# Optimization experiments

Hardware: AMD Instinct MI355X
Metric: run time of the kernel (lower is better)

## Reference

```python
import jax, jax.numpy as jnp
import numpy as np

KNN = 5
SEARCH = 3
CUTOFF = 1.0
NCLASSES = 21
D, H, W = 32, 128, 2048
P = 1048576


def setup_inputs() -> dict:
    key = jax.random.key(0)
    k1, k2, k3, k4, k5, k6 = jax.random.split(key, 6)
    proj_range = jax.random.uniform(k1, (D, H, W), dtype=jnp.float32)
    unproj_range = jax.random.uniform(k2, (P,), dtype=jnp.float32)
    proj_argmax = jax.random.randint(k3, (D, H, W), 0, NCLASSES).astype(jnp.int32)
    px = jax.random.randint(k4, (P,), 0, W).astype(jnp.int32)
    py = jax.random.randint(k5, (P,), 0, H).astype(jnp.int32)
    pz = jax.random.randint(k6, (P,), 0, D).astype(jnp.int32)
    return {"proj_range": proj_range, "unproj_range": unproj_range,
            "proj_argmax": proj_argmax, "px": px, "py": py, "pz": pz}


def reference(proj_range, unproj_range, proj_argmax, px, py, pz):
    pad = (SEARCH - 1) // 2
    k3 = SEARCH ** 3
    center = (k3 - 1) // 2  # = 13 for search=3
    n_pts = unproj_range.shape[0]

    # zero padding replicates F.unfold's implicit zero pad (padded entries stay 0,
    # which is NOT mapped to inf by the `< 0` mask, matching the torch code)
    pr_pad = jnp.pad(proj_range, pad)
    pa_pad = jnp.pad(proj_argmax, pad)

    # kernel offsets, flattened in (dz, dy, dx) order like unfoldNd
    offs = jnp.arange(SEARCH, dtype=jnp.int32)
    oz, oy, ox = jnp.meshgrid(offs, offs, offs, indexing="ij")
    oz, oy, ox = oz.reshape(-1), oy.reshape(-1), ox.reshape(-1)  # [k3]

    # per-point neighborhood indices into the padded volume: [P, k3]
    zi = pz[:, None] + oz[None, :]
    yi = py[:, None] + oy[None, :]
    xi = px[:, None] + ox[None, :]

    nb_rang = pr_pad[zi, yi, xi]                       # [P, k3]
    nb_rang = jnp.where(nb_rang < 0, jnp.inf, nb_rang)
    nb_rang = nb_rang.at[:, center].set(unproj_range)  # center = query range

    k2_dist = jnp.abs(nb_rang - unproj_range[:, None])  # [P, k3]

    neg_top, knn_idx = jax.lax.top_k(-k2_dist, KNN)     # smallest-k distances
    knn_dist = -neg_top                                  # [P, KNN]

    nb_arg = pa_pad[zi, yi, xi]                          # [P, k3] int
    knn_arg = jnp.take_along_axis(nb_arg, knn_idx, axis=1)
    knn_arg = jnp.where(knn_dist > CUTOFF, NCLASSES, knn_arg)  # cutoff -> invalid class

    # scatter-add voting over classes 0..NCLASSES
    counts = jnp.zeros((n_pts, NCLASSES + 1), dtype=proj_range.dtype)
    counts = counts.at[jnp.arange(n_pts, dtype=jnp.int32)[:, None], knn_arg].add(1.0)

    # argmax over classes 1..NCLASSES-1 (drop class 0 and invalid bucket), then +1
    out = jnp.argmax(counts[:, 1:-1], axis=1).astype(jnp.int32) + 1
    return out
```

## Files before the change

kernel.cpp:

```cpp
#include <hip/hip_runtime.h>
#include <math.h>

#define KNN 5
#define K3 27
#define CENTER 13
#define NCLASSES 21
#define DIM_D 32
#define DIM_H 128
#define DIM_W 2048

#define RADIX 256
#define BIN_PTS 2048
#define SEG_TILE 2048


typedef float    float4u __attribute__((ext_vector_type(4), aligned(4)));
typedef int      int4u   __attribute__((ext_vector_type(4), aligned(4)));
typedef unsigned uint2u  __attribute__((ext_vector_type(2), aligned(4)));
typedef unsigned uint4e  __attribute__((ext_vector_type(4), aligned(16)));

#define SENTINEL 3.0e38f
#define BITS_TWO 0x4000000000000000ULL

__device__ __forceinline__ unsigned seg_of_xy(int x, int y) {
    return ((unsigned)y << 1) | ((unsigned)x >> 10);
}
__device__ __forceinline__ unsigned seg_of_wy(unsigned wy) {
    return (((wy >> 11) & 0x7Fu) << 1) | ((wy >> 10) & 1u);
}
__device__ __forceinline__ unsigned b8_of_wy(unsigned wy) {
    return (((wy >> 18) & 31u) << 3) | ((wy >> 7) & 7u);
}

__global__ __launch_bounds__(256) void pack_pa_kernel(
    const int4* __restrict__ pa, uchar4* __restrict__ out, int n4)
{
    int i = blockIdx.x * 256 + threadIdx.x;
    if (i < n4) {
        int4 v = pa[i];
        out[i] = make_uchar4((unsigned char)v.x, (unsigned char)v.y,
                             (unsigned char)v.z, (unsigned char)v.w);
    }
}

__global__ __launch_bounds__(256) void hist0_kernel(
    const int* __restrict__ px, const int* __restrict__ py,
    unsigned* __restrict__ h0, int P)
{
    __shared__ unsigned lh0[RADIX];
    int t = threadIdx.x;
    lh0[t] = 0;
    __syncthreads();
    int base4 = blockIdx.x * 1024 + t;
#pragma unroll
    for (int g = 0; g < 4; ++g) {
        int i4 = base4 + g * 256;
        int i0 = i4 * 4;
        if (i0 + 3 < P) {
            int4 X = ((const int4*)px)[i4];
            int4 Y = ((const int4*)py)[i4];
            atomicAdd(&lh0[seg_of_xy(X.x, Y.x)], 1u);
            atomicAdd(&lh0[seg_of_xy(X.y, Y.y)], 1u);
            atomicAdd(&lh0[seg_of_xy(X.z, Y.z)], 1u);
            atomicAdd(&lh0[seg_of_xy(X.w, Y.w)], 1u);
        } else {
            for (int i = i0; i < P; ++i)
                atomicAdd(&lh0[seg_of_xy(px[i], py[i])], 1u);
        }
    }
    __syncthreads();
    if (lh0[t]) atomicAdd(&h0[t], lh0[t]);
}

__global__ __launch_bounds__(256) void scan256_dup_kernel(
    unsigned* __restrict__ h, unsigned* __restrict__ hbase)
{
    __shared__ unsigned ws[4];
    int t = threadIdx.x, lane = t & 63, wid = t >> 6;
    unsigned a = h[t], ia = a;
#pragma unroll
    for (int off = 1; off < 64; off <<= 1) {
        unsigned v = __shfl_up(ia, off);
        if (lane >= off) ia += v;
    }
    if (lane == 63) ws[wid] = ia;
    __syncthreads();
    unsigned b = 0;
#pragma unroll
    for (int w = 0; w < 4; ++w) b += (w < wid) ? ws[w] : 0u;
    unsigned excl = b + ia - a;
    h[t] = excl;
    hbase[t] = excl;
}

struct BinShared {
    unsigned lh[RADIX];
    unsigned lscan[RADIX];
    unsigned gbase[RADIX];
    unsigned wsum[4];
    uint4 stage[BIN_PTS];
};

__global__ __launch_bounds__(512) void bin_pass1_kernel(
    const float* __restrict__ ur, const int* __restrict__ px,
    const int* __restrict__ py, const int* __restrict__ pz,
    unsigned* __restrict__ g0, uint4* __restrict__ outp, int P)
{
    __shared__ BinShared S;
    int t = threadIdx.x, lane = t & 63, wid = t >> 6;
    int bstart = blockIdx.x * BIN_PTS;
    int n = min(BIN_PTS, P - bstart);
    if (t < RADIX) S.lh[t] = 0;
    __syncthreads();

    uint4 pay[4];
    unsigned rk[4], dg[4];
    {
        int i4 = (bstart >> 2) + t;
        int i0 = i4 * 4;
        if (i0 + 3 < P) {
            int4 X = ((const int4*)px)[i4];
            int4 Y = ((const int4*)py)[i4];
            int4 Z = ((const int4*)pz)[i4];
            float4 U = ((const float4*)ur)[i4];
            int xs[4] = {X.x, X.y, X.z, X.w};
            int ys[4] = {Y.x, Y.y, Y.z, Y.w};
            int zs[4] = {Z.x, Z.y, Z.z, Z.w};
            float us[4] = {U.x, U.y, U.z, U.w};
#pragma unroll
            for (int c = 0; c < 4; ++c) {
                dg[c] = seg_of_xy(xs[c], ys[c]);
                rk[c] = atomicAdd(&S.lh[dg[c]], 1u);
                pay[c] = make_uint4(__float_as_uint(us[c]),
                    (unsigned)xs[c] | ((unsigned)ys[c] << 11) | ((unsigned)zs[c] << 18),
                    (unsigned)(i0 + c), 0u);
            }
        } else {
#pragma unroll
            for (int c = 0; c < 4; ++c) {
                int gi = i0 + c;
                if (gi < P) {
                    int x = px[gi], y = py[gi], z = pz[gi];
                    dg[c] = seg_of_xy(x, y);
                    rk[c] = atomicAdd(&S.lh[dg[c]], 1u);
                    pay[c] = make_uint4(__float_as_uint(ur[gi]),
                        (unsigned)x | ((unsigned)y << 11) | ((unsigned)z << 18),
                        (unsigned)gi, 0u);
                } else {
                    dg[c] = 0xFFFFFFFFu;
                }
            }
        }
    }
    __syncthreads();

    {
        unsigned c0 = (t < RADIX) ? S.lh[t] : 0u;
        unsigned inc = c0;
#pragma unroll
        for (int off = 1; off < 64; off <<= 1) {
            unsigned v = __shfl_up(inc, off);
            if (lane >= off) inc += v;
        }
        if (t < RADIX && lane == 63) S.wsum[wid] = inc;
        __syncthreads();
        if (t < RADIX) {
            unsigned wb = 0;
#pragma unroll
            for (int w = 0; w < 4; ++w) wb += (w < wid) ? S.wsum[w] : 0u;
            S.lscan[t] = wb + inc - c0;
            S.gbase[t] = c0 ? atomicAdd(&g0[t], c0) : 0u;
        }
    }
    __syncthreads();
#pragma unroll
    for (int c = 0; c < 4; ++c)
        if (dg[c] != 0xFFFFFFFFu)
            S.stage[S.lscan[dg[c]] + rk[c]] = pay[c];
    __syncthreads();
#pragma unroll
    for (int j = 0; j < 4; ++j) {
        int s = j * 512 + t;
        if (s < n) {
            uint4 v = S.stage[s];
            unsigned d = seg_of_wy(v.y);
            unsigned pos = S.gbase[d] + ((unsigned)s - S.lscan[d]);
            outp[pos] = v;
        }
    }
}

__global__ __launch_bounds__(1024) void pass2b_kernel(
    const uint4* __restrict__ inp, const unsigned* __restrict__ segBase,
    uint4* __restrict__ outp, int P)
{
    __shared__ unsigned bh[RADIX];
    __shared__ unsigned cur[RADIX];
    __shared__ unsigned lz[RADIX];
    __shared__ unsigned lsc[RADIX];
    __shared__ unsigned wsum[4];
    __shared__ uint4 stage[SEG_TILE];

    int b = blockIdx.x;
    unsigned s0 = segBase[b];
    unsigned s1 = (b == RADIX - 1) ? (unsigned)P : segBase[b + 1];
    int t = threadIdx.x, lane = t & 63, wid = t >> 6;

    if (t < RADIX) bh[t] = 0;
    __syncthreads();

    for (unsigned i = s0 + t; i < s1; i += 1024)
        atomicAdd(&bh[b8_of_wy(inp[i].y)], 1u);
    __syncthreads();

    {
        unsigned c0 = (t < RADIX) ? bh[t] : 0u;
        unsigned inc = c0;
#pragma unroll
        for (int off = 1; off < 64; off <<= 1) {
            unsigned v = __shfl_up(inc, off);
            if (lane >= off) inc += v;
        }
        if (t < RADIX && lane == 63) wsum[wid] = inc;
        __syncthreads();
        if (t < RADIX) {
            unsigned wb = 0;
#pragma unroll
            for (int w = 0; w < 4; ++w) wb += (w < wid) ? wsum[w] : 0u;
            cur[t] = s0 + wb + inc - c0;
        }
    }
    __syncthreads();

    for (unsigned tb = s0; tb < s1; tb += SEG_TILE) {
        unsigned m = min((unsigned)SEG_TILE, s1 - tb);
        if (t < RADIX) lz[t] = 0;
        __syncthreads();
        uint4 pay[2];
        unsigned rk[2], zz[2];
#pragma unroll
        for (int j = 0; j < 2; ++j) {
            int s = j * 1024 + t;
            if (s < (int)m) {
                uint4 v = inp[tb + (unsigned)s];
                pay[j] = v;
                zz[j] = b8_of_wy(v.y);
                rk[j] = atomicAdd(&lz[zz[j]], 1u);
            } else {
                zz[j] = 0xFFFFFFFFu;
            }
        }
        __syncthreads();
        {
            unsigned c0 = (t < RADIX) ? lz[t] : 0u;
            unsigned inc = c0;
#pragma unroll
            for (int off = 1; off < 64; off <<= 1) {
                unsigned v = __shfl_up(inc, off);
                if (lane >= off) inc += v;
            }
            if (t < RADIX && lane == 63) wsum[wid] = inc;
            __syncthreads();
            if (t < RADIX) {
                unsigned wb = 0;
#pragma unroll
                for (int w = 0; w < 4; ++w) wb += (w < wid) ? wsum[w] : 0u;
                lsc[t] = wb + inc - c0;
            }
        }
        __syncthreads();
#pragma unroll
        for (int j = 0; j < 2; ++j)
            if (zz[j] != 0xFFFFFFFFu)
                stage[lsc[zz[j]] + rk[j]] = pay[j];
        __syncthreads();
#pragma unroll
        for (int j = 0; j < 2; ++j) {
            int s = j * 1024 + t;
            if (s < (int)m) {
                uint4 v = stage[s];
                unsigned d = b8_of_wy(v.y);
                outp[cur[d] + ((unsigned)s - lsc[d])] = v;
            }
        }
        __syncthreads();
        if (t < RADIX) cur[t] += lz[t];
        __syncthreads();
    }
}

template <bool U8>
__device__ __forceinline__ void bev_knn_body(
    const float* __restrict__ pr, const int* __restrict__ pa,
    const unsigned char* __restrict__ pa8,
    float u, int x, int y, int z, int oidx, int* __restrict__ out)
{
    int xo = min(max(x - 1, 0), DIM_W - 4);
    int s = x - 1 - xo;
    int xo8 = (max(x - 1, 0)) & ~3;
    int sb = (x - 1) - xo8;

    float4u L[9];
    int4u   A[9];
    uint2u  B[9];
    bool okr[9];
#pragma unroll
    for (int r = 0; r < 9; ++r) {
        const int dz = r / 3 - 1;
        const int dy = r % 3 - 1;
        int zz = z + dz, yy = y + dy;
        bool ok = ((unsigned)zz < (unsigned)DIM_D) &
                  ((unsigned)yy < (unsigned)DIM_H);
        okr[r] = ok;
        int row = ok ? (zz * DIM_H + yy) : 0;
        size_t rb = ((size_t)row) << 11;
        L[r] = *(const float4u*)(pr + rb + xo);
        if (U8) B[r] = *(const uint2u*)(pa8 + rb + xo8);
        else    A[r] = *(const int4u*)(pa + rb + xo);
    }

    double bd[KNN];
#pragma unroll
    for (int j = 0; j < KNN; ++j) bd[j] = 1.0e308;

    auto push = [&](int k, float v, unsigned cls) {
        float d = fabsf(v - u);
        d = (v < 0.f) ? SENTINEL : d;
        if (k == CENTER) d = 0.0f;
        double key = (double)d + 1.0;
        unsigned long long kb =
            (unsigned long long)__double_as_longlong(key)
            | (unsigned long long)(((unsigned)k << 5) | (cls & 31u));
        double kd = __longlong_as_double((long long)kb);
#pragma unroll
        for (int j = 0; j < KNN; ++j) {
            double lo = fmin(bd[j], kd);
            kd = fmax(bd[j], kd);
            bd[j] = lo;
        }
    };

    bool fast = __all(s == 0);
    if (fast) {
#pragma unroll
        for (int r = 0; r < 9; ++r) {
            bool ok = okr[r];
            float v0, v1, v2;
            unsigned cc0, cc1, cc2;
            v0 = ok ? L[r].x : 0.f;
            v1 = ok ? L[r].y : 0.f;
            v2 = ok ? L[r].z : 0.f;
            if (U8) {
                unsigned long long v64 =
                    ((unsigned long long)B[r].y << 32) | B[r].x;
                unsigned c3 = ok ? (unsigned)(v64 >> (8 * sb)) : 0u;
                cc0 = c3 & 0xFFu;
                cc1 = (c3 >> 8) & 0xFFu;
                cc2 = (c3 >> 16) & 0xFFu;
            } else {
                cc0 = ok ? (unsigned)A[r].x : 0u;
                cc1 = ok ? (unsigned)A[r].y : 0u;
                cc2 = ok ? (unsigned)A[r].z : 0u;
            }
            push(r * 3 + 0, v0, cc0);
            push(r * 3 + 1, v1, cc1);
            push(r * 3 + 2, v2, cc2);
        }
    } else {
#pragma unroll
        for (int r = 0; r < 9; ++r) {
            bool ok = okr[r];
            float a0 = ok ? L[r].x : 0.f;
            float a1 = ok ? L[r].y : 0.f;
            float a2 = ok ? L[r].z : 0.f;
            float a3 = ok ? L[r].w : 0.f;
            float v0 = (s == 0) ? a0 : ((s == -1) ? 0.f : ((s == 1) ? a1 : a2));
            float v1 = (s == 0) ? a1 : ((s == -1) ? a0 : ((s == 1) ? a2 : a3));
            float v2 = (s == 0) ? a2 : ((s == -1) ? a1 : ((s == 1) ? a3 : 0.f));
            unsigned cv[3];
            if (U8) {
                unsigned long long v64 = ok ?
                    (((unsigned long long)B[r].y << 32) | B[r].x) : 0ULL;
#pragma unroll
                for (int j = 0; j < 3; ++j) {
                    int xm = x - 1 + j;
                    bool xv = (unsigned)xm < (unsigned)DIM_W;
                    int idx = sb + j;
                    idx = idx < 0 ? 0 : idx;
                    unsigned byte = (unsigned)((v64 >> (8 * idx)) & 0xFFu);
                    cv[j] = xv ? byte : 0u;
                }
            } else {
                unsigned c0 = ok ? (unsigned)A[r].x : 0u;
                unsigned c1 = ok ? (unsigned)A[r].y : 0u;
                unsigned c2 = ok ? (unsigned)A[r].z : 0u;
                unsigned c3 = ok ? (unsigned)A[r].w : 0u;
                cv[0] = (s == 0) ? c0 : ((s == -1) ? 0u : ((s == 1) ? c1 : c2));
                cv[1] = (s == 0) ? c1 : ((s == -1) ? c0 : ((s == 1) ? c2 : c3));
                cv[2] = (s == 0) ? c2 : ((s == -1) ? c1 : ((s == 1) ? c3 : 0u));
            }
            push(r * 3 + 0, v0, cv[0]);
            push(r * 3 + 1, v1, cv[1]);
            push(r * 3 + 2, v2, cv[2]);
        }
    }

    int votes[KNN];
#pragma unroll
    for (int j = 0; j < KNN; ++j) {
        unsigned long long kb =
            (unsigned long long)__double_as_longlong(bd[j]);
        int cls = (int)(kb & 31u);
        bool cut = (kb & ~1023ULL) > BITS_TWO;
        votes[j] = cut ? NCLASSES : cls;
    }

    int best_cnt = 0, best_cls = 1;
#pragma unroll
    for (int j = 0; j < KNN; ++j) {
        int v = votes[j];
        if (v >= 1 && v <= NCLASSES - 1) {
            int cnt = 0;
#pragma unroll
            for (int i = 0; i < KNN; ++i) cnt += (votes[i] == v) ? 1 : 0;
            if (cnt > best_cnt || (cnt == best_cnt && v < best_cls)) {
                best_cnt = cnt;
                best_cls = v;
            }
        }
    }
    __builtin_nontemporal_store(best_cls, &out[oidx]);
}

__device__ __forceinline__ int swizzle_block(int b, int nb) {
    if ((nb & 7) == 0) {
        int per = nb >> 3;
        return (b & 7) * per + (b >> 3);
    }
    return b;
}

template <bool U8>
__global__ __launch_bounds__(256) void bev_knn_aos_kernel(
    const float* __restrict__ pr, const int* __restrict__ pa,
    const unsigned char* __restrict__ pa8,
    const uint4* __restrict__ payload, int* __restrict__ out, int P)
{
    int lb = swizzle_block(blockIdx.x, gridDim.x);
    int p = lb * blockDim.x + threadIdx.x;
    if (p >= P) return;
    uint4e w = __builtin_nontemporal_load((const uint4e*)(payload + p));
    float u = __uint_as_float(w.x);
    int x = (int)(w.y & 0x7FFu);
    int y = (int)((w.y >> 11) & 0x7Fu);
    int z = (int)((w.y >> 18) & 0x1Fu);
    bev_knn_body<U8>(pr, pa, pa8, u, x, y, z, (int)w.z, out);
}

__global__ __launch_bounds__(256) void bev_knn_direct_kernel(
    const float* __restrict__ pr, const int* __restrict__ pa,
    const float* __restrict__ ur, const int* __restrict__ px,
    const int* __restrict__ py, const int* __restrict__ pz,
    int* __restrict__ out, int P)
{
    int p = blockIdx.x * blockDim.x + threadIdx.x;
    if (p >= P) return;
    bev_knn_body<false>(pr, pa, (const unsigned char*)nullptr,
                        ur[p], px[p], py[p], pz[p], p, out);
}

extern "C" void kernel_launch(void* const* d_in, const int* in_sizes, int n_in,
                              void* d_out, int out_size, void* d_ws, size_t ws_size,
                              hipStream_t stream) {
    const float* pr = (const float*)d_in[0];
    const float* ur = (const float*)d_in[1];
    const int*   pa = (const int*)d_in[2];
    const int*   px = (const int*)d_in[3];
    const int*   py = (const int*)d_in[4];
    const int*   pz = (const int*)d_in[5];
    int* out = (int*)d_out;
    int P = in_sizes[1];
    int gridH = (P + 4095) / 4096;
    int gridB = (P + BIN_PTS - 1) / BIN_PTS;
    int gridD = (P + 255) / 256;

    const int VOXELS = DIM_D * DIM_H * DIM_W;
    size_t h_b    = (size_t)RADIX * 4;
    size_t hb_b   = (size_t)RADIX * 4;
    size_t p_off  = (h_b + hb_b + 15) & ~(size_t)15;
    size_t pay_b  = (size_t)P * 16;
    size_t need   = p_off + 2 * pay_b;
    size_t pack_b = ((size_t)VOXELS + 31) & ~(size_t)31;
    size_t need8  = need + pack_b;

    if (ws_size >= need) {
        char* ws = (char*)d_ws;
        unsigned* h0cur  = (unsigned*)ws;
        unsigned* h0base = (unsigned*)(ws + h_b);
        uint4*    pay1   = (uint4*)(ws + p_off);
        uint4*    pay2   = (uint4*)(ws + p_off + pay_b);
        unsigned char* pa8 = (unsigned char*)(ws + p_off + 2 * pay_b);
        bool use8 = (ws_size >= need8);

        hipMemsetAsync(h0cur, 0, h_b, stream);
        if (use8) {
            int n4 = VOXELS / 4;
            pack_pa_kernel<<<(n4 + 255) / 256, 256, 0, stream>>>(
                (const int4*)pa, (uchar4*)pa8, n4);
        }
        hist0_kernel<<<gridH, 256, 0, stream>>>(px, py, h0cur, P);
        scan256_dup_kernel<<<1, 256, 0, stream>>>(h0cur, h0base);
        bin_pass1_kernel<<<gridB, 512, 0, stream>>>(ur, px, py, pz,
                                                    h0cur, pay1, P);
        pass2b_kernel<<<RADIX, 1024, 0, stream>>>(pay1, h0base, pay2, P);
        if (use8)
            bev_knn_aos_kernel<true><<<gridD, 256, 0, stream>>>(
                pr, pa, pa8, pay2, out, P);
        else
            bev_knn_aos_kernel<false><<<gridD, 256, 0, stream>>>(
                pr, pa, nullptr, pay2, out, P);
    } else {
        bev_knn_direct_kernel<<<gridD, 256, 0, stream>>>(pr, pa, ur, px, py,
                                                         pz, out, P);
    }
}
```

Measured before the change: 180.5 us.

## Fuse pack, histogram and scan into one kernel; precompute second-level bin counts

Merges the int-to-byte argmax packing, the first-level segment histogram and the 256-entry scan into a single prep kernel. A last-block-done atomic counter runs the scan, which removes two kernel launches. The first binning pass now also builds the second-level 256x256 histogram with global atomics, so pass2b no longer rereads its whole segment just to count sub-bins. The cost is one global atomic per point on a 256 KB count table and a larger workspace memset.

```diff
diff --git a/kernel.cpp b/kernel.cpp
--- a/kernel.cpp
+++ b/kernel.cpp
@@ -32,65 +32,70 @@
     return (((wy >> 18) & 31u) << 3) | ((wy >> 7) & 7u);
 }
 
-__global__ __launch_bounds__(256) void pack_pa_kernel(
-    const int4* __restrict__ pa, uchar4* __restrict__ out, int n4)
+__global__ __launch_bounds__(256) void prep_kernel(
+    const int4* __restrict__ pa, uchar4* __restrict__ pa8,
+    const int* __restrict__ px, const int* __restrict__ py,
+    unsigned* __restrict__ h0, unsigned* __restrict__ hbase,
+    unsigned* __restrict__ done, int n4, int P, int histBlocks)
 {
-    int i = blockIdx.x * 256 + threadIdx.x;
+    __shared__ unsigned lh0[RADIX];
+    __shared__ unsigned sws[4];
+    __shared__ bool isLast;
+    int t = threadIdx.x;
+    int b = blockIdx.x;
+
+    int i = b * 256 + t;
     if (i < n4) {
         int4 v = pa[i];
-        out[i] = make_uchar4((unsigned char)v.x, (unsigned char)v.y,
+        pa8[i] = make_uchar4((unsigned char)v.x, (unsigned char)v.y,
                              (unsigned char)v.z, (unsigned char)v.w);
     }
-}
-
-__global__ __launch_bounds__(256) void hist0_kernel(
-    const int* __restrict__ px, const int* __restrict__ py,
-    unsigned* __restrict__ h0, int P)
-{
-    __shared__ unsigned lh0[RADIX];
-    int t = threadIdx.x;
-    lh0[t] = 0;
-    __syncthreads();
-    int base4 = blockIdx.x * 1024 + t;
-#pragma unroll
-    for (int g = 0; g < 4; ++g) {
-        int i4 = base4 + g * 256;
-        int i0 = i4 * 4;
-        if (i0 + 3 < P) {
-            int4 X = ((const int4*)px)[i4];
-            int4 Y = ((const int4*)py)[i4];
-            atomicAdd(&lh0[seg_of_xy(X.x, Y.x)], 1u);
-            atomicAdd(&lh0[seg_of_xy(X.y, Y.y)], 1u);
-            atomicAdd(&lh0[seg_of_xy(X.z, Y.z)], 1u);
-            atomicAdd(&lh0[seg_of_xy(X.w, Y.w)], 1u);
-        } else {
-            for (int i = i0; i < P; ++i)
-                atomicAdd(&lh0[seg_of_xy(px[i], py[i])], 1u);
-        }
-    }
-    __syncthreads();
-    if (lh0[t]) atomicAdd(&h0[t], lh0[t]);
-}
-
-__global__ __launch_bounds__(256) void scan256_dup_kernel(
-    unsigned* __restrict__ h, unsigned* __restrict__ hbase)
-{
-    __shared__ unsigned ws[4];
-    int t = threadIdx.x, lane = t & 63, wid = t >> 6;
-    unsigned a = h[t], ia = a;
-#pragma unroll
-    for (int off = 1; off < 64; off <<= 1) {
-        unsigned v = __shfl_up(ia, off);
-        if (lane >= off) ia += v;
-    }
-    if (lane == 63) ws[wid] = ia;
-    __syncthreads();
-    unsigned b = 0;
-#pragma unroll
-    for (int w = 0; w < 4; ++w) b += (w < wid) ? ws[w] : 0u;
-    unsigned excl = b + ia - a;
-    h[t] = excl;
-    hbase[t] = excl;
+
+    if (b < histBlocks) {
+        lh0[t] = 0;
+        __syncthreads();
+        int base4 = b * 1024 + t;
+#pragma unroll
+        for (int g = 0; g < 4; ++g) {
+            int i4 = base4 + g * 256;
+            int i0 = i4 * 4;
+            if (i0 + 3 < P) {
+                int4 X = ((const int4*)px)[i4];
+                int4 Y = ((const int4*)py)[i4];
+                atomicAdd(&lh0[seg_of_xy(X.x, Y.x)], 1u);
+                atomicAdd(&lh0[seg_of_xy(X.y, Y.y)], 1u);
+                atomicAdd(&lh0[seg_of_xy(X.z, Y.z)], 1u);
+                atomicAdd(&lh0[seg_of_xy(X.w, Y.w)], 1u);
+            } else {
+                for (int j = i0; j < P; ++j)
+                    atomicAdd(&lh0[seg_of_xy(px[j], py[j])], 1u);
+            }
+        }
+        __syncthreads();
+        if (lh0[t]) atomicAdd(&h0[t], lh0[t]);
+    }
+
+    __syncthreads();
+    if (t == 0)
+        isLast = (atomicAdd(done, 1u) == (unsigned)(gridDim.x - 1));
+    __syncthreads();
+    if (isLast) {
+        int lane = t & 63, wid = t >> 6;
+        unsigned a = atomicAdd(&h0[t], 0u), ia = a;
+#pragma unroll
+        for (int off = 1; off < 64; off <<= 1) {
+            unsigned v = __shfl_up(ia, off);
+            if (lane >= off) ia += v;
+        }
+        if (lane == 63) sws[wid] = ia;
+        __syncthreads();
+        unsigned bb = 0;
+#pragma unroll
+        for (int w = 0; w < 4; ++w) bb += (w < wid) ? sws[w] : 0u;
+        unsigned excl = bb + ia - a;
+        h0[t] = excl;
+        hbase[t] = excl;
+    }
 }
 
 struct BinShared {
@@ -104,7 +109,8 @@
 __global__ __launch_bounds__(512) void bin_pass1_kernel(
     const float* __restrict__ ur, const int* __restrict__ px,
     const int* __restrict__ py, const int* __restrict__ pz,
-    unsigned* __restrict__ g0, uint4* __restrict__ outp, int P)
+    unsigned* __restrict__ g0, unsigned* __restrict__ cnt16,
+    uint4* __restrict__ outp, int P)
 {
     __shared__ BinShared S;
     int t = threadIdx.x, lane = t & 63, wid = t >> 6;
@@ -134,6 +140,7 @@
                 pay[c] = make_uint4(__float_as_uint(us[c]),
                     (unsigned)xs[c] | ((unsigned)ys[c] << 11) | ((unsigned)zs[c] << 18),
                     (unsigned)(i0 + c), 0u);
+                atomicAdd(&cnt16[(dg[c] << 8) | b8_of_wy(pay[c].y)], 1u);
             }
         } else {
 #pragma unroll
@@ -146,6 +153,7 @@
                     pay[c] = make_uint4(__float_as_uint(ur[gi]),
                         (unsigned)x | ((unsigned)y << 11) | ((unsigned)z << 18),
                         (unsigned)gi, 0u);
+                    atomicAdd(&cnt16[(dg[c] << 8) | b8_of_wy(pay[c].y)], 1u);
                 } else {
                     dg[c] = 0xFFFFFFFFu;
                 }
@@ -192,9 +200,8 @@
 
 __global__ __launch_bounds__(1024) void pass2b_kernel(
     const uint4* __restrict__ inp, const unsigned* __restrict__ segBase,
-    uint4* __restrict__ outp, int P)
+    const unsigned* __restrict__ cnt16, uint4* __restrict__ outp, int P)
 {
-    __shared__ unsigned bh[RADIX];
     __shared__ unsigned cur[RADIX];
     __shared__ unsigned lz[RADIX];
     __shared__ unsigned lsc[RADIX];
@@ -206,15 +213,8 @@
     unsigned s1 = (b == RADIX - 1) ? (unsigned)P : segBase[b + 1];
     int t = threadIdx.x, lane = t & 63, wid = t >> 6;
 
-    if (t < RADIX) bh[t] = 0;
-    __syncthreads();
-
-    for (unsigned i = s0 + t; i < s1; i += 1024)
-        atomicAdd(&bh[b8_of_wy(inp[i].y)], 1u);
-    __syncthreads();
-
     {
-        unsigned c0 = (t < RADIX) ? bh[t] : 0u;
+        unsigned c0 = (t < RADIX) ? cnt16[(b << 8) | t] : 0u;
         unsigned inc = c0;
 #pragma unroll
         for (int off = 1; off < 64; off <<= 1) {
@@ -480,16 +480,18 @@
     const int*   pz = (const int*)d_in[5];
     int* out = (int*)d_out;
     int P = in_sizes[1];
-    int gridH = (P + 4095) / 4096;
     int gridB = (P + BIN_PTS - 1) / BIN_PTS;
     int gridD = (P + 255) / 256;
+    int histBlocks = (P + 4095) / 4096;
 
     const int VOXELS = DIM_D * DIM_H * DIM_W;
     size_t h_b    = (size_t)RADIX * 4;
     size_t hb_b   = (size_t)RADIX * 4;
-    size_t p_off  = (h_b + hb_b + 15) & ~(size_t)15;
+    size_t done_b = 16;
+    size_t cnt_b  = (size_t)RADIX * RADIX * 4;
+    size_t pre    = (h_b + hb_b + done_b + cnt_b + 255) & ~(size_t)255;
     size_t pay_b  = (size_t)P * 16;
-    size_t need   = p_off + 2 * pay_b;
+    size_t need   = pre + 2 * pay_b;
     size_t pack_b = ((size_t)VOXELS + 31) & ~(size_t)31;
     size_t need8  = need + pack_b;
 
@@ -497,22 +499,25 @@
         char* ws = (char*)d_ws;
         unsigned* h0cur  = (unsigned*)ws;
         unsigned* h0base = (unsigned*)(ws + h_b);
-        uint4*    pay1   = (uint4*)(ws + p_off);
-        uint4*    pay2   = (uint4*)(ws + p_off + pay_b);
-        unsigned char* pa8 = (unsigned char*)(ws + p_off + 2 * pay_b);
+        unsigned* done   = (unsigned*)(ws + h_b + hb_b);
+        unsigned* cnt16  = (unsigned*)(ws + h_b + hb_b + done_b);
+        uint4*    pay1   = (uint4*)(ws + pre);
+        uint4*    pay2   = (uint4*)(ws + pre + pay_b);
+        unsigned char* pa8 = (unsigned char*)(ws + pre + 2 * pay_b);
         bool use8 = (ws_size >= need8);
 
-        hipMemsetAsync(h0cur, 0, h_b, stream);
-        if (use8) {
-            int n4 = VOXELS / 4;
-            pack_pa_kernel<<<(n4 + 255) / 256, 256, 0, stream>>>(
-                (const int4*)pa, (uchar4*)pa8, n4);
-        }
-        hist0_kernel<<<gridH, 256, 0, stream>>>(px, py, h0cur, P);
-        scan256_dup_kernel<<<1, 256, 0, stream>>>(h0cur, h0base);
+        hipMemsetAsync(ws, 0, pre, stream);
+
+        int n4 = use8 ? (VOXELS / 4) : 0;
+        int packBlocks = use8 ? (n4 + 255) / 256 : 0;
+        int gridP = max(packBlocks, histBlocks);
+        prep_kernel<<<gridP, 256, 0, stream>>>(
+            (const int4*)pa, (uchar4*)pa8, px, py,
+            h0cur, h0base, done, n4, P, histBlocks);
         bin_pass1_kernel<<<gridB, 512, 0, stream>>>(ur, px, py, pz,
-                                                    h0cur, pay1, P);
-        pass2b_kernel<<<RADIX, 1024, 0, stream>>>(pay1, h0base, pay2, P);
+                                                    h0cur, cnt16, pay1, P);
+        pass2b_kernel<<<RADIX, 1024, 0, stream>>>(pay1, h0base, cnt16,
+                                                  pay2, P);
         if (use8)
             bev_knn_aos_kernel<true><<<gridD, 256, 0, stream>>>(
                 pr, pa, pa8, pay2, out, P);
```

Result: slower. 293.8 us (+62.8%).

## Convert sorted point payload from padded AoS uint4 to three SoA arrays

Applied to the files above, without the earlier changes.

The 16-byte per-point payload (range, packed xyz, index, unused pad) is replaced by three separate 4-byte arrays across both binning passes and the KNN kernel. This drops the unused fourth word, cutting intermediate payload traffic by a quarter, and gives coalesced 4-byte accesses. The cost is three separate scattered stores per point instead of one 16-byte store, plus more LDS staging arrays and extra memory instructions. The workspace layout is adjusted to match.

```diff
diff --git a/kernel.cpp b/kernel.cpp
--- a/kernel.cpp
+++ b/kernel.cpp
@@ -17,7 +17,6 @@
 typedef float    float4u __attribute__((ext_vector_type(4), aligned(4)));
 typedef int      int4u   __attribute__((ext_vector_type(4), aligned(4)));
 typedef unsigned uint2u  __attribute__((ext_vector_type(2), aligned(4)));
-typedef unsigned uint4e  __attribute__((ext_vector_type(4), aligned(16)));
 
 #define SENTINEL 3.0e38f
 #define BITS_TWO 0x4000000000000000ULL
@@ -98,13 +97,17 @@
     unsigned lscan[RADIX];
     unsigned gbase[RADIX];
     unsigned wsum[4];
-    uint4 stage[BIN_PTS];
+    unsigned stW[BIN_PTS];
+    unsigned stU[BIN_PTS];
+    unsigned stI[BIN_PTS];
 };
 
 __global__ __launch_bounds__(512) void bin_pass1_kernel(
     const float* __restrict__ ur, const int* __restrict__ px,
     const int* __restrict__ py, const int* __restrict__ pz,
-    unsigned* __restrict__ g0, uint4* __restrict__ outp, int P)
+    unsigned* __restrict__ g0,
+    unsigned* __restrict__ oW, unsigned* __restrict__ oU,
+    unsigned* __restrict__ oI, int P)
 {
     __shared__ BinShared S;
     int t = threadIdx.x, lane = t & 63, wid = t >> 6;
@@ -113,8 +116,7 @@
     if (t < RADIX) S.lh[t] = 0;
     __syncthreads();
 
-    uint4 pay[4];
-    unsigned rk[4], dg[4];
+    unsigned pw[4], pu[4], rk[4], dg[4];
     {
         int i4 = (bstart >> 2) + t;
         int i0 = i4 * 4;
@@ -131,9 +133,9 @@
             for (int c = 0; c < 4; ++c) {
                 dg[c] = seg_of_xy(xs[c], ys[c]);
                 rk[c] = atomicAdd(&S.lh[dg[c]], 1u);
-                pay[c] = make_uint4(__float_as_uint(us[c]),
-                    (unsigned)xs[c] | ((unsigned)ys[c] << 11) | ((unsigned)zs[c] << 18),
-                    (unsigned)(i0 + c), 0u);
+                pw[c] = (unsigned)xs[c] | ((unsigned)ys[c] << 11)
+                        | ((unsigned)zs[c] << 18);
+                pu[c] = __float_as_uint(us[c]);
             }
         } else {
 #pragma unroll
@@ -143,9 +145,9 @@
                     int x = px[gi], y = py[gi], z = pz[gi];
                     dg[c] = seg_of_xy(x, y);
                     rk[c] = atomicAdd(&S.lh[dg[c]], 1u);
-                    pay[c] = make_uint4(__float_as_uint(ur[gi]),
-                        (unsigned)x | ((unsigned)y << 11) | ((unsigned)z << 18),
-                        (unsigned)gi, 0u);
+                    pw[c] = (unsigned)x | ((unsigned)y << 11)
+                            | ((unsigned)z << 18);
+                    pu[c] = __float_as_uint(ur[gi]);
                 } else {
                     dg[c] = 0xFFFFFFFFu;
                 }
@@ -173,33 +175,47 @@
         }
     }
     __syncthreads();
+    {
+        int i0 = bstart + t * 4 - t * 3;
+        (void)i0;
+    }
 #pragma unroll
     for (int c = 0; c < 4; ++c)
-        if (dg[c] != 0xFFFFFFFFu)
-            S.stage[S.lscan[dg[c]] + rk[c]] = pay[c];
+        if (dg[c] != 0xFFFFFFFFu) {
+            unsigned sl = S.lscan[dg[c]] + rk[c];
+            S.stW[sl] = pw[c];
+            S.stU[sl] = pu[c];
+            S.stI[sl] = (unsigned)(((bstart >> 2) + t) * 4 + c);
+        }
     __syncthreads();
 #pragma unroll
     for (int j = 0; j < 4; ++j) {
         int s = j * 512 + t;
         if (s < n) {
-            uint4 v = S.stage[s];
-            unsigned d = seg_of_wy(v.y);
+            unsigned wv = S.stW[s];
+            unsigned d = seg_of_wy(wv);
             unsigned pos = S.gbase[d] + ((unsigned)s - S.lscan[d]);
-            outp[pos] = v;
+            oW[pos] = wv;
+            oU[pos] = S.stU[s];
+            oI[pos] = S.stI[s];
         }
     }
 }
 
 __global__ __launch_bounds__(1024) void pass2b_kernel(
-    const uint4* __restrict__ inp, const unsigned* __restrict__ segBase,
-    uint4* __restrict__ outp, int P)
+    const unsigned* __restrict__ iW, const unsigned* __restrict__ iU,
+    const unsigned* __restrict__ iI, const unsigned* __restrict__ segBase,
+    unsigned* __restrict__ oW, unsigned* __restrict__ oU,
+    unsigned* __restrict__ oI, int P)
 {
     __shared__ unsigned bh[RADIX];
     __shared__ unsigned cur[RADIX];
     __shared__ unsigned lz[RADIX];
     __shared__ unsigned lsc[RADIX];
     __shared__ unsigned wsum[4];
-    __shared__ uint4 stage[SEG_TILE];
+    __shared__ unsigned stW[SEG_TILE];
+    __shared__ unsigned stU[SEG_TILE];
+    __shared__ unsigned stI[SEG_TILE];
 
     int b = blockIdx.x;
     unsigned s0 = segBase[b];
@@ -210,7 +226,7 @@
     __syncthreads();
 
     for (unsigned i = s0 + t; i < s1; i += 1024)
-        atomicAdd(&bh[b8_of_wy(inp[i].y)], 1u);
+        atomicAdd(&bh[b8_of_wy(iW[i])], 1u);
     __syncthreads();
 
     {
@@ -236,15 +252,16 @@
         unsigned m = min((unsigned)SEG_TILE, s1 - tb);
         if (t < RADIX) lz[t] = 0;
         __syncthreads();
-        uint4 pay[2];
-        unsigned rk[2], zz[2];
+        unsigned vw[2], vu[2], vi[2], rk[2], zz[2];
 #pragma unroll
         for (int j = 0; j < 2; ++j) {
             int s = j * 1024 + t;
             if (s < (int)m) {
-                uint4 v = inp[tb + (unsigned)s];
-                pay[j] = v;
-                zz[j] = b8_of_wy(v.y);
+                unsigned gi = tb + (unsigned)s;
+                vw[j] = iW[gi];
+                vu[j] = iU[gi];
+                vi[j] = iI[gi];
+                zz[j] = b8_of_wy(vw[j]);
                 rk[j] = atomicAdd(&lz[zz[j]], 1u);
             } else {
                 zz[j] = 0xFFFFFFFFu;
@@ -271,16 +288,23 @@
         __syncthreads();
 #pragma unroll
         for (int j = 0; j < 2; ++j)
-            if (zz[j] != 0xFFFFFFFFu)
-                stage[lsc[zz[j]] + rk[j]] = pay[j];
+            if (zz[j] != 0xFFFFFFFFu) {
+                unsigned sl = lsc[zz[j]] + rk[j];
+                stW[sl] = vw[j];
+                stU[sl] = vu[j];
+                stI[sl] = vi[j];
+            }
         __syncthreads();
 #pragma unroll
         for (int j = 0; j < 2; ++j) {
             int s = j * 1024 + t;
             if (s < (int)m) {
-                uint4 v = stage[s];
-                unsigned d = b8_of_wy(v.y);
-                outp[cur[d] + ((unsigned)s - lsc[d])] = v;
+                unsigned wv = stW[s];
+                unsigned d = b8_of_wy(wv);
+                unsigned pos = cur[d] + ((unsigned)s - lsc[d]);
+                oW[pos] = wv;
+                oU[pos] = stU[s];
+                oI[pos] = stI[s];
             }
         }
         __syncthreads();
@@ -444,17 +468,20 @@
 __global__ __launch_bounds__(256) void bev_knn_aos_kernel(
     const float* __restrict__ pr, const int* __restrict__ pa,
     const unsigned char* __restrict__ pa8,
-    const uint4* __restrict__ payload, int* __restrict__ out, int P)
+    const unsigned* __restrict__ pW, const unsigned* __restrict__ pU,
+    const unsigned* __restrict__ pI, int* __restrict__ out, int P)
 {
     int lb = swizzle_block(blockIdx.x, gridDim.x);
     int p = lb * blockDim.x + threadIdx.x;
     if (p >= P) return;
-    uint4e w = __builtin_nontemporal_load((const uint4e*)(payload + p));
-    float u = __uint_as_float(w.x);
-    int x = (int)(w.y & 0x7FFu);
-    int y = (int)((w.y >> 11) & 0x7Fu);
-    int z = (int)((w.y >> 18) & 0x1Fu);
-    bev_knn_body<U8>(pr, pa, pa8, u, x, y, z, (int)w.z, out);
+    unsigned wv = __builtin_nontemporal_load(pW + p);
+    unsigned uv = __builtin_nontemporal_load(pU + p);
+    unsigned iv = __builtin_nontemporal_load(pI + p);
+    float u = __uint_as_float(uv);
+    int x = (int)(wv & 0x7FFu);
+    int y = (int)((wv >> 11) & 0x7Fu);
+    int z = (int)((wv >> 18) & 0x1Fu);
+    bev_knn_body<U8>(pr, pa, pa8, u, x, y, z, (int)iv, out);
 }
 
 __global__ __launch_bounds__(256) void bev_knn_direct_kernel(
@@ -487,9 +514,9 @@
     const int VOXELS = DIM_D * DIM_H * DIM_W;
     size_t h_b    = (size_t)RADIX * 4;
     size_t hb_b   = (size_t)RADIX * 4;
-    size_t p_off  = (h_b + hb_b + 15) & ~(size_t)15;
-    size_t pay_b  = (size_t)P * 16;
-    size_t need   = p_off + 2 * pay_b;
+    size_t pre    = (h_b + hb_b + 255) & ~(size_t)255;
+    size_t arr_b  = ((size_t)P * 4 + 255) & ~(size_t)255;
+    size_t need   = pre + 6 * arr_b;
     size_t pack_b = ((size_t)VOXELS + 31) & ~(size_t)31;
     size_t need8  = need + pack_b;
 
@@ -497,12 +524,17 @@
         char* ws = (char*)d_ws;
         unsigned* h0cur  = (unsigned*)ws;
         unsigned* h0base = (unsigned*)(ws + h_b);
-        uint4*    pay1   = (uint4*)(ws + p_off);
-        uint4*    pay2   = (uint4*)(ws + p_off + pay_b);
-        unsigned char* pa8 = (unsigned char*)(ws + p_off + 2 * pay_b);
+        unsigned* p1W = (unsigned*)(ws + pre);
+        unsigned* p1U = (unsigned*)(ws + pre + arr_b);
+        unsigned* p1I = (unsigned*)(ws + pre + 2 * arr_b);
+        unsigned* p2W = (unsigned*)(ws + pre + 3 * arr_b);
+        unsigned* p2U = (unsigned*)(ws + pre + 4 * arr_b);
+        unsigned* p2I = (unsigned*)(ws + pre + 5 * arr_b);
+        unsigned char* pa8 = (unsigned char*)(ws + pre + 6 * arr_b);
         bool use8 = (ws_size >= need8);
 
-        hipMemsetAsync(h0cur, 0, h_b, stream);
+        hipMemsetAsync(ws, 0, pre, stream);
+
         if (use8) {
             int n4 = VOXELS / 4;
             pack_pa_kernel<<<(n4 + 255) / 256, 256, 0, stream>>>(
@@ -510,15 +542,16 @@
         }
         hist0_kernel<<<gridH, 256, 0, stream>>>(px, py, h0cur, P);
         scan256_dup_kernel<<<1, 256, 0, stream>>>(h0cur, h0base);
-        bin_pass1_kernel<<<gridB, 512, 0, stream>>>(ur, px, py, pz,
-                                                    h0cur, pay1, P);
-        pass2b_kernel<<<RADIX, 1024, 0, stream>>>(pay1, h0base, pay2, P);
+        bin_pass1_kernel<<<gridB, 512, 0, stream>>>(ur, px, py, pz, h0cur,
+                                                    p1W, p1U, p1I, P);
+        pass2b_kernel<<<RADIX, 1024, 0, stream>>>(p1W, p1U, p1I, h0base,
+                                                  p2W, p2U, p2I, P);
         if (use8)
             bev_knn_aos_kernel<true><<<gridD, 256, 0, stream>>>(
-                pr, pa, pa8, pay2, out, P);
+                pr, pa, pa8, p2W, p2U, p2I, out, P);
         else
             bev_knn_aos_kernel<false><<<gridD, 256, 0, stream>>>(
-                pr, pa, nullptr, pay2, out, P);
+                pr, pa, nullptr, p2W, p2U, p2I, out, P);
     } else {
         bev_knn_direct_kernel<<<gridD, 256, 0, stream>>>(pr, pa, ur, px, py,
                                                          pz, out, P);
```

New measurement: 183.5 us. Within noise of the previous version (+1.7%).
